# Performance work log

Measured on AMD Instinct MI355X. Metric: run time of the kernel, lower is better.

Reference implementation:

```python
import jax, jax.numpy as jnp
import numpy as np

D = 1024
H = 16
HD = D // H
EPS = 1e-5

def _ln(t, gamma, beta):
    # LayerNorm over last dim (head_dim)
    mu = jnp.mean(t, axis=-1, keepdims=True)
    var = jnp.mean(jnp.square(t - mu), axis=-1, keepdims=True)
    return (t - mu) * jax.lax.rsqrt(var + EPS) * gamma + beta

def setup_inputs() -> dict:
    key = jax.random.key(0)
    ks = jax.random.split(key, 6)
    B, S = 2, 2048
    # xavier_uniform bound for square [D,D] weight
    bound = float(np.sqrt(6.0 / (D + D)))
    x = jax.random.normal(ks[0], (B, S, D), dtype=jnp.float32)
    Wq = jax.random.uniform(ks[1], (D, D), jnp.float32, -bound, bound)
    Wk = jax.random.uniform(ks[2], (D, D), jnp.float32, -bound, bound)
    Wv = jax.random.uniform(ks[3], (D, D), jnp.float32, -bound, bound)
    Wp = jax.random.uniform(ks[4], (D, D), jnp.float32, -bound, bound)
    bp = jnp.zeros((D,), jnp.float32)
    gq = jnp.ones((HD,), jnp.float32); bq = jnp.zeros((HD,), jnp.float32)
    gk = jnp.ones((HD,), jnp.float32); bk = jnp.zeros((HD,), jnp.float32)
    return {"x": x, "Wq": Wq, "Wk": Wk, "Wv": Wv, "Wp": Wp, "bp": bp,
            "gq": gq, "bq": bq, "gk": gk, "bk": bk}

def reference(x, Wq, Wk, Wv, Wp, bp, gq, bq, gk, bk):
    B, S, _ = x.shape
    scale = HD ** -0.5
    # torch Linear: x @ W.T -> (B,S,H,HD) -> (B,H,S,HD)
    q = (x @ Wq.T).reshape(B, S, H, HD).transpose(0, 2, 1, 3)
    k = (x @ Wk.T).reshape(B, S, H, HD).transpose(0, 2, 1, 3)
    v = (x @ Wv.T).reshape(B, S, H, HD).transpose(0, 2, 1, 3)
    q = _ln(q, gq, bq)
    k = _ln(k, gk, bk)
    scores = jnp.einsum('bhqd,bhkd->bhqk', q, k) * scale
    causal_mask = jnp.triu(jnp.ones((S, S), dtype=bool), k=1)  # True above diagonal
    scores = jnp.where(causal_mask[None, None], -jnp.inf, scores)
    attn = jax.nn.softmax(scores, axis=-1)
    out = jnp.einsum('bhqk,bhkd->bhqd', attn, v).transpose(0, 2, 1, 3).reshape(B, S, D)
    out = out @ Wp.T + bp
    return (out, attn)
```

## Files before the change

### kernel.cpp

```cpp
#include <hip/hip_runtime.h>

typedef _Float16 f16;
typedef _Float16 f16x4 __attribute__((ext_vector_type(4)));
typedef _Float16 f16x8 __attribute__((ext_vector_type(8)));
typedef float f32x4 __attribute__((ext_vector_type(4)));

#define D_ 1024
#define H_ 16
#define HD_ 64
#define B_ 2
#define S_ 2048
#define M_ 4096
#define SCALE 0.125f
#define NEG_BIG -1e30f

__device__ __forceinline__ float red16_sum(float v) {
#pragma unroll
  for (int m = 8; m >= 1; m >>= 1) v += __shfl_xor(v, m);
  return v;
}

__device__ __forceinline__ void gload16(const f16* g, f16* l) {
  __builtin_amdgcn_global_load_lds((const __attribute__((address_space(1))) void*)g,
                                   (__attribute__((address_space(3))) void*)l, 16, 0, 0);
}

__global__ __launch_bounds__(256) void k_cvt5(const float* __restrict__ x,
    const float* __restrict__ w0, const float* __restrict__ w1,
    const float* __restrict__ w2, const float* __restrict__ w3,
    f16* __restrict__ xh, f16* __restrict__ wh)
{
  const int y = blockIdx.y;
  const float* src; f16* dst; int n4;
  if (y == 0) { src = x; dst = xh; n4 = (M_ * D_) / 4; }
  else {
    src = (y == 1) ? w0 : (y == 2) ? w1 : (y == 3) ? w2 : w3;
    dst = wh + (size_t)(y - 1) * D_ * D_;
    n4 = (D_ * D_) / 4;
  }
  const int stride = gridDim.x * blockDim.x;
  for (int i = blockIdx.x * blockDim.x + threadIdx.x; i < n4; i += stride) {
    f32x4 v = ((const f32x4*)src)[i];
    ((f16x4*)dst)[i] = (f16x4){(f16)v[0], (f16)v[1], (f16)v[2], (f16)v[3]};
  }
}

__device__ __forceinline__ void gemm128(const f16* __restrict__ A, const f16* __restrict__ Bw,
                                        int K, int bm, int bn, f32x4 acc[4][4])
{
  __shared__ f16 As[128][64];
  __shared__ f16 Bs[128][64];
  const int tid = threadIdx.x;
  const int lane = tid & 63, wid = tid >> 6;
  const int wr = wid >> 1, wc = wid & 1, g = lane >> 4, li = lane & 15;
  const int lrow = lane >> 3, lcol = (lane & 7) * 8;

#pragma unroll
  for (int m = 0; m < 4; ++m)
#pragma unroll
    for (int n = 0; n < 4; ++n)
      acc[m][n] = (f32x4){0.f, 0.f, 0.f, 0.f};

  for (int k0 = 0; k0 < K; k0 += 64) {
#pragma unroll
    for (int i = 0; i < 4; ++i) {
      int c = wid * 4 + i;
      int row = c * 8 + lrow;
      gload16(&A[(size_t)(bm + row) * K + k0 + lcol], &As[c * 8][0]);
      gload16(&Bw[(size_t)(bn + row) * K + k0 + lcol], &Bs[c * 8][0]);
    }
    __syncthreads();
#pragma unroll
    for (int kk = 0; kk < 64; kk += 32) {
      f16x8 af[4], bf[4];
#pragma unroll
      for (int m = 0; m < 4; ++m) af[m] = *(const f16x8*)&As[wr * 64 + m * 16 + li][kk + g * 8];
#pragma unroll
      for (int n = 0; n < 4; ++n) bf[n] = *(const f16x8*)&Bs[wc * 64 + n * 16 + li][kk + g * 8];
#pragma unroll
      for (int m = 0; m < 4; ++m)
#pragma unroll
        for (int n = 0; n < 4; ++n)
          acc[m][n] = __builtin_amdgcn_mfma_f32_16x16x32_f16(af[m], bf[n], acc[m][n], 0, 0, 0);
    }
    __syncthreads();
  }
}

__global__ __launch_bounds__(256) void k_gemm_qkv(const f16* __restrict__ xh,
    const f16* __restrict__ wh,
    const float* __restrict__ gq, const float* __restrict__ bq,
    const float* __restrict__ gk, const float* __restrict__ bk,
    f16* __restrict__ qt, f16* __restrict__ kt, f16* __restrict__ vh)
{
  const int z = blockIdx.z;
  const f16* Bw = wh + (size_t)z * D_ * D_;
  f16* C = (z == 0) ? qt : (z == 1) ? kt : vh;
  f32x4 acc[4][4];
  gemm128(xh, Bw, D_, blockIdx.x * 128, blockIdx.y * 128, acc);
  const int tid = threadIdx.x, lane = tid & 63, wid = tid >> 6;
  const int wr = wid >> 1, wc = wid & 1, g = lane >> 4, li = lane & 15;
  const int hh = blockIdx.y * 2 + wc;
  const float* gamma = (z == 0) ? gq : gk;
  const float* beta  = (z == 0) ? bq : bk;
  float gm[4], bt[4];
  if (z < 2) {
#pragma unroll
    for (int n = 0; n < 4; ++n) { gm[n] = gamma[n * 16 + li]; bt[n] = beta[n * 16 + li]; }
  }
#pragma unroll
  for (int m = 0; m < 4; ++m)
#pragma unroll
    for (int r = 0; r < 4; ++r) {
      int rr = blockIdx.x * 128 + wr * 64 + m * 16 + g * 4 + r;
      int b = rr >> 11, s = rr & (S_ - 1);
      float v0 = acc[m][0][r], v1 = acc[m][1][r], v2 = acc[m][2][r], v3 = acc[m][3][r];
      if (z < 2) {
        float mean = red16_sum(v0 + v1 + v2 + v3) * (1.f / 64.f);
        v0 -= mean; v1 -= mean; v2 -= mean; v3 -= mean;
        float ss = red16_sum(v0 * v0 + v1 * v1 + v2 * v2 + v3 * v3);
        float inv = rsqrtf(ss * (1.f / 64.f) + 1e-5f);
        v0 = v0 * inv * gm[0] + bt[0]; v1 = v1 * inv * gm[1] + bt[1];
        v2 = v2 * inv * gm[2] + bt[2]; v3 = v3 * inv * gm[3] + bt[3];
      }
      f16* dst = C + ((size_t)(b * H_ + hh) * S_ + s) * HD_;
      dst[li]      = (f16)v0;
      dst[16 + li] = (f16)v1;
      dst[32 + li] = (f16)v2;
      dst[48 + li] = (f16)v3;
    }
}

__global__ __launch_bounds__(256) void k_gemm_proj(const f16* __restrict__ oh,
    const f16* __restrict__ Wph, const float* __restrict__ bp, float* __restrict__ out)
{
  f32x4 acc[4][4];
  gemm128(oh, Wph, D_, blockIdx.x * 128, blockIdx.y * 128, acc);
  const int tid = threadIdx.x, lane = tid & 63, wid = tid >> 6;
  const int wr = wid >> 1, wc = wid & 1, g = lane >> 4, li = lane & 15;
#pragma unroll
  for (int m = 0; m < 4; ++m)
#pragma unroll
    for (int n = 0; n < 4; ++n)
#pragma unroll
      for (int r = 0; r < 4; ++r) {
        int rr = blockIdx.x * 128 + wr * 64 + m * 16 + g * 4 + r;
        int cc = blockIdx.y * 128 + wc * 64 + n * 16 + li;
        out[(size_t)rr * D_ + cc] = acc[m][n][r] + bp[cc];
      }
}

__global__ __launch_bounds__(256) void k_transpose_v(const f16* __restrict__ vh, f16* __restrict__ vt)
{
  __shared__ f16 T[64][72];
  const int tid = threadIdx.x;
  const int s0 = blockIdx.x * 64, h = blockIdx.y, b = blockIdx.z;
  const f16* src = vh + ((size_t)(b * H_ + h) * S_ + s0) * HD_;
#pragma unroll
  for (int i = 0; i < 2; ++i) {
    int slot = tid + i * 256, sl = slot >> 3, ch = (slot & 7) * 8;
    *(f16x8*)&T[sl][ch] = *(const f16x8*)&src[(size_t)sl * HD_ + ch];
  }
  __syncthreads();
#pragma unroll
  for (int i = 0; i < 2; ++i) {
    int slot = tid + i * 256, d = slot >> 3, sc = (slot & 7) * 8;
    f16x8 val;
#pragma unroll
    for (int j = 0; j < 8; ++j) val[j] = T[sc + j][d];
    *(f16x8*)&vt[((size_t)(b * H_ + h) * HD_ + d) * S_ + s0 + sc] = val;
  }
}

__global__ __launch_bounds__(64, 2) void k_attn_fused(const f16* __restrict__ qt,
    const f16* __restrict__ kt, const f16* __restrict__ vt,
    float* __restrict__ attn, f16* __restrict__ oh)
{
  __shared__ f16 Ps[32][138];
  const int bx = blockIdx.x;
  const int bh = bx & 31;
  const int s  = 63 - (bx >> 5);
  const int b = bh >> 4, h = bh & 15;
  const int lane = threadIdx.x;
  const int g = lane >> 4, li = lane & 15;
  const int row0 = s * 32;
  const int ntk = (s + 4) >> 2;
  const f16* Qb = qt + (size_t)bh * S_ * HD_;
  const f16* Kb = kt + (size_t)bh * S_ * HD_;
  float* attnB = attn + (size_t)bh * S_ * S_;

  f16x8 qa[2][2];
#pragma unroll
  for (int m = 0; m < 2; ++m)
#pragma unroll
    for (int kk = 0; kk < 2; ++kk)
      qa[m][kk] = *(const f16x8*)&Qb[(size_t)(row0 + m * 16 + li) * HD_ + kk * 32 + g * 8];

  float lrun[2][4];
#pragma unroll
  for (int m = 0; m < 2; ++m)
#pragma unroll
    for (int r = 0; r < 4; ++r) lrun[m][r] = 0.f;

  for (int tk = 0; tk < ntk; ++tk) {
    const bool diag = (tk == ntk - 1);
#pragma unroll
    for (int nh = 0; nh < 2; ++nh) {
      f32x4 acc[2][4];
#pragma unroll
      for (int m = 0; m < 2; ++m)
#pragma unroll
        for (int j = 0; j < 4; ++j) acc[m][j] = (f32x4){0.f, 0.f, 0.f, 0.f};
#pragma unroll
      for (int kk = 0; kk < 2; ++kk) {
        f16x8 kf[4];
#pragma unroll
        for (int j = 0; j < 4; ++j)
          kf[j] = *(const f16x8*)&Kb[(size_t)(tk * 128 + nh * 64 + j * 16 + li) * HD_ + kk * 32 + g * 8];
#pragma unroll
        for (int m = 0; m < 2; ++m)
#pragma unroll
          for (int j = 0; j < 4; ++j)
            acc[m][j] = __builtin_amdgcn_mfma_f32_16x16x32_f16(qa[m][kk], kf[j], acc[m][j], 0, 0, 0);
      }
#pragma unroll
      for (int m = 0; m < 2; ++m)
#pragma unroll
        for (int r = 0; r < 4; ++r) {
          int row = row0 + m * 16 + g * 4 + r;
#pragma unroll
          for (int j = 0; j < 4; ++j) {
            float sv = acc[m][j][r] * SCALE;
            if (diag) { int col = tk * 128 + nh * 64 + j * 16 + li; if (col > row) sv = NEG_BIG; }
            lrun[m][r] += __expf(sv);
          }
        }
    }
  }
  float il[2][4];
#pragma unroll
  for (int m = 0; m < 2; ++m)
#pragma unroll
    for (int r = 0; r < 4; ++r) il[m][r] = 1.f / red16_sum(lrun[m][r]);

  f32x4 oacc[2][4];
#pragma unroll
  for (int m = 0; m < 2; ++m)
#pragma unroll
    for (int n = 0; n < 4; ++n) oacc[m][n] = (f32x4){0.f, 0.f, 0.f, 0.f};

  for (int tk = 0; tk < ntk; ++tk) {
    const bool diag = (tk == ntk - 1);
#pragma unroll
    for (int nh = 0; nh < 2; ++nh) {
      f32x4 acc[2][4];
#pragma unroll
      for (int m = 0; m < 2; ++m)
#pragma unroll
        for (int j = 0; j < 4; ++j) acc[m][j] = (f32x4){0.f, 0.f, 0.f, 0.f};
#pragma unroll
      for (int kk = 0; kk < 2; ++kk) {
        f16x8 kf[4];
#pragma unroll
        for (int j = 0; j < 4; ++j)
          kf[j] = *(const f16x8*)&Kb[(size_t)(tk * 128 + nh * 64 + j * 16 + li) * HD_ + kk * 32 + g * 8];
#pragma unroll
        for (int m = 0; m < 2; ++m)
#pragma unroll
          for (int j = 0; j < 4; ++j)
            acc[m][j] = __builtin_amdgcn_mfma_f32_16x16x32_f16(qa[m][kk], kf[j], acc[m][j], 0, 0, 0);
      }
#pragma unroll
      for (int m = 0; m < 2; ++m)
#pragma unroll
        for (int r = 0; r < 4; ++r) {
          int row = row0 + m * 16 + g * 4 + r;
          float* rowp = attnB + (size_t)row * S_ + tk * 128 + nh * 64 + li;
#pragma unroll
          for (int j = 0; j < 4; ++j) {
            float sv = acc[m][j][r] * SCALE;
            if (diag) { int col = tk * 128 + nh * 64 + j * 16 + li; if (col > row) sv = NEG_BIG; }
            float p = __expf(sv) * il[m][r];
            __builtin_nontemporal_store(p, rowp + j * 16);
            Ps[m * 16 + g * 4 + r][nh * 64 + j * 16 + li] = (f16)p;
          }
        }
    }
#pragma unroll
    for (int kk = 0; kk < 4; ++kk) {
      f16x8 vbf[4];
#pragma unroll
      for (int n = 0; n < 4; ++n)
        vbf[n] = *(const f16x8*)&vt[((size_t)bh * HD_ + n * 16 + li) * S_ + tk * 128 + kk * 32 + g * 8];
#pragma unroll
      for (int m = 0; m < 2; ++m) {
        f16x8 pa = *(const f16x8*)&Ps[m * 16 + li][kk * 32 + g * 8];
#pragma unroll
        for (int n = 0; n < 4; ++n)
          oacc[m][n] = __builtin_amdgcn_mfma_f32_16x16x32_f16(pa, vbf[n], oacc[m][n], 0, 0, 0);
      }
    }
  }

  {
    const int zr = lane >> 5, zc = (lane & 31) * 4;
    f32x4 z = {0.f, 0.f, 0.f, 0.f};
    for (int tk = ntk; tk < 16; ++tk) {
      float* a0 = attnB + (size_t)row0 * S_ + tk * 128;
#pragma unroll
      for (int rr = 0; rr < 32; rr += 2)
        __builtin_nontemporal_store(z, (f32x4*)(a0 + (size_t)(rr + zr) * S_ + zc));
    }
  }

#pragma unroll
  for (int m = 0; m < 2; ++m)
#pragma unroll
    for (int n = 0; n < 4; ++n)
#pragma unroll
      for (int r = 0; r < 4; ++r)
        oh[(size_t)(b * S_ + row0 + m * 16 + g * 4 + r) * D_ + h * HD_ + n * 16 + li] = (f16)oacc[m][n][r];
}

extern "C" void kernel_launch(void* const* d_in, const int* in_sizes, int n_in,
                              void* d_out, int out_size, void* d_ws, size_t ws_size,
                              hipStream_t stream)
{
  (void)in_sizes; (void)n_in; (void)out_size; (void)ws_size;
  const float* x  = (const float*)d_in[0];
  const float* Wq = (const float*)d_in[1];
  const float* Wk = (const float*)d_in[2];
  const float* Wv = (const float*)d_in[3];
  const float* Wp = (const float*)d_in[4];
  const float* bp = (const float*)d_in[5];
  const float* gq = (const float*)d_in[6];
  const float* bq = (const float*)d_in[7];
  const float* gk = (const float*)d_in[8];
  const float* bk = (const float*)d_in[9];

  float* out  = (float*)d_out;
  float* attn = out + (size_t)B_ * S_ * D_;

  f16* xh  = (f16*)d_ws;
  f16* wh  = xh + (size_t)M_ * D_;
  f16* qt  = wh + (size_t)4 * D_ * D_;
  f16* kt  = qt + (size_t)M_ * D_;
  f16* vh  = kt + (size_t)M_ * D_;
  f16* vt  = vh + (size_t)M_ * D_;
  f16* oh  = vt + (size_t)M_ * D_;

  dim3 blk(256);
  k_cvt5<<<dim3(256, 5), blk, 0, stream>>>(x, Wq, Wk, Wv, Wp, xh, wh);
  k_gemm_qkv<<<dim3(32, 8, 3), blk, 0, stream>>>(xh, wh, gq, bq, gk, bk, qt, kt, vh);
  k_transpose_v<<<dim3(32, 16, 2), blk, 0, stream>>>(vh, vt);
  k_attn_fused<<<dim3(2048), dim3(64), 0, stream>>>(qt, kt, vt, attn, oh);
  k_gemm_proj<<<dim3(32, 8), blk, 0, stream>>>(oh, wh + (size_t)3 * D_ * D_, bp, out);
}
```

Measured before the change: 302.4 us.

## Split attention key tiles across two waves per block with LDS reduction

```diff
diff --git a/kernel.cpp b/kernel.cpp
--- a/kernel.cpp
+++ b/kernel.cpp
@@ -172,19 +172,23 @@
   }
 }
 
-__global__ __launch_bounds__(64, 2) void k_attn_fused(const f16* __restrict__ qt,
+__global__ __launch_bounds__(128, 4) void k_attn_fused(const f16* __restrict__ qt,
     const f16* __restrict__ kt, const f16* __restrict__ vt,
     float* __restrict__ attn, f16* __restrict__ oh)
 {
-  __shared__ f16 Ps[32][138];
+  __shared__ f16 Ps[2][32][138];
+  __shared__ float Ls[2][32];
   const int bx = blockIdx.x;
   const int bh = bx & 31;
   const int s  = 63 - (bx >> 5);
   const int b = bh >> 4, h = bh & 15;
-  const int lane = threadIdx.x;
+  const int tid = threadIdx.x;
+  const int wid = tid >> 6, lane = tid & 63;
   const int g = lane >> 4, li = lane & 15;
   const int row0 = s * 32;
   const int ntk = (s + 4) >> 2;
+  const int tmid = (ntk + 1) >> 1;
+  const int t0 = wid ? tmid : 0, t1 = wid ? ntk : tmid;
   const f16* Qb = qt + (size_t)bh * S_ * HD_;
   const f16* Kb = kt + (size_t)bh * S_ * HD_;
   float* attnB = attn + (size_t)bh * S_ * S_;
@@ -202,7 +206,7 @@
 #pragma unroll
     for (int r = 0; r < 4; ++r) lrun[m][r] = 0.f;
 
-  for (int tk = 0; tk < ntk; ++tk) {
+  for (int tk = t0; tk < t1; ++tk) {
     const bool diag = (tk == ntk - 1);
 #pragma unroll
     for (int nh = 0; nh < 2; ++nh) {
@@ -237,11 +241,22 @@
         }
     }
   }
+#pragma unroll
+  for (int m = 0; m < 2; ++m)
+#pragma unroll
+    for (int r = 0; r < 4; ++r) {
+      lrun[m][r] = red16_sum(lrun[m][r]);
+      if (li == 0) Ls[wid][m * 16 + g * 4 + r] = lrun[m][r];
+    }
+  __syncthreads();
   float il[2][4];
 #pragma unroll
   for (int m = 0; m < 2; ++m)
 #pragma unroll
-    for (int r = 0; r < 4; ++r) il[m][r] = 1.f / red16_sum(lrun[m][r]);
+    for (int r = 0; r < 4; ++r) {
+      int idx = m * 16 + g * 4 + r;
+      il[m][r] = 1.f / (Ls[0][idx] + Ls[1][idx]);
+    }
 
   f32x4 oacc[2][4];
 #pragma unroll
@@ -249,7 +264,7 @@
 #pragma unroll
     for (int n = 0; n < 4; ++n) oacc[m][n] = (f32x4){0.f, 0.f, 0.f, 0.f};
 
-  for (int tk = 0; tk < ntk; ++tk) {
+  for (int tk = t0; tk < t1; ++tk) {
     const bool diag = (tk == ntk - 1);
 #pragma unroll
     for (int nh = 0; nh < 2; ++nh) {
@@ -282,7 +297,7 @@
             if (diag) { int col = tk * 128 + nh * 64 + j * 16 + li; if (col > row) sv = NEG_BIG; }
             float p = __expf(sv) * il[m][r];
             __builtin_nontemporal_store(p, rowp + j * 16);
-            Ps[m * 16 + g * 4 + r][nh * 64 + j * 16 + li] = (f16)p;
+            Ps[wid][m * 16 + g * 4 + r][nh * 64 + j * 16 + li] = (f16)p;
           }
         }
     }
@@ -294,7 +309,7 @@
         vbf[n] = *(const f16x8*)&vt[((size_t)bh * HD_ + n * 16 + li) * S_ + tk * 128 + kk * 32 + g * 8];
 #pragma unroll
       for (int m = 0; m < 2; ++m) {
-        f16x8 pa = *(const f16x8*)&Ps[m * 16 + li][kk * 32 + g * 8];
+        f16x8 pa = *(const f16x8*)&Ps[wid][m * 16 + li][kk * 32 + g * 8];
 #pragma unroll
         for (int n = 0; n < 4; ++n)
           oacc[m][n] = __builtin_amdgcn_mfma_f32_16x16x32_f16(pa, vbf[n], oacc[m][n], 0, 0, 0);
@@ -305,7 +320,7 @@
   {
     const int zr = lane >> 5, zc = (lane & 31) * 4;
     f32x4 z = {0.f, 0.f, 0.f, 0.f};
-    for (int tk = ntk; tk < 16; ++tk) {
+    for (int tk = ntk + wid; tk < 16; tk += 2) {
       float* a0 = attnB + (size_t)row0 * S_ + tk * 128;
 #pragma unroll
       for (int rr = 0; rr < 32; rr += 2)
@@ -313,13 +328,29 @@
     }
   }
 
-#pragma unroll
-  for (int m = 0; m < 2; ++m)
-#pragma unroll
-    for (int n = 0; n < 4; ++n)
-#pragma unroll
-      for (int r = 0; r < 4; ++r)
-        oh[(size_t)(b * S_ + row0 + m * 16 + g * 4 + r) * D_ + h * HD_ + n * 16 + li] = (f16)oacc[m][n][r];
+  __syncthreads();
+  float* Os = (float*)&Ps[0][0][0];
+  if (wid == 1) {
+#pragma unroll
+    for (int m = 0; m < 2; ++m)
+#pragma unroll
+      for (int n = 0; n < 4; ++n)
+#pragma unroll
+        for (int r = 0; r < 4; ++r)
+          Os[(m * 16 + g * 4 + r) * 64 + n * 16 + li] = oacc[m][n][r];
+  }
+  __syncthreads();
+  if (wid == 0) {
+#pragma unroll
+    for (int m = 0; m < 2; ++m)
+#pragma unroll
+      for (int n = 0; n < 4; ++n)
+#pragma unroll
+        for (int r = 0; r < 4; ++r) {
+          float v = oacc[m][n][r] + Os[(m * 16 + g * 4 + r) * 64 + n * 16 + li];
+          oh[(size_t)(b * S_ + row0 + m * 16 + g * 4 + r) * D_ + h * HD_ + n * 16 + li] = (f16)v;
+        }
+  }
 }
 
 extern "C" void kernel_launch(void* const* d_in, const int* in_sizes, int n_in,
@@ -353,6 +384,6 @@
   k_cvt5<<<dim3(256, 5), blk, 0, stream>>>(x, Wq, Wk, Wv, Wp, xh, wh);
   k_gemm_qkv<<<dim3(32, 8, 3), blk, 0, stream>>>(xh, wh, gq, bq, gk, bk, qt, kt, vh);
   k_transpose_v<<<dim3(32, 16, 2), blk, 0, stream>>>(vh, vt);
-  k_attn_fused<<<dim3(2048), dim3(64), 0, stream>>>(qt, kt, vt, attn, oh);
+  k_attn_fused<<<dim3(2048), dim3(128), 0, stream>>>(qt, kt, vt, attn, oh);
   k_gemm_proj<<<dim3(32, 8), blk, 0, stream>>>(oh, wh + (size_t)3 * D_ * D_, bp, out);
 }
```

Result: slower. 322.0 us (+6.5%).
